# Kernel optimization log

Hardware: AMD Instinct MI355X
Metric: run time of the kernel (lower is better)

The kernel has to match this reference:

```python
import jax, jax.numpy as jnp
import numpy as np

NUM_HEADS = 8
HEAD_DIM = 32  # token_dim 256 / 8 heads


def setup_inputs() -> dict:
    key = jax.random.key(0)
    ks = jax.random.split(key, 12)
    Q, N, E, D, G = 8192, 65536, 262144, 256, 64
    query_tokens = jax.random.normal(ks[0], (Q, D), dtype=jnp.float32)
    support_feats = jax.random.normal(ks[1], (N, D), dtype=jnp.float32)
    geo_embed = jax.random.normal(ks[2], (Q, G), dtype=jnp.float32)
    q_idx = jnp.sort(jax.random.randint(ks[3], (E,), 0, Q, dtype=jnp.int32)).astype(jnp.int32)
    s_idx = jax.random.randint(ks[4], (E,), 0, N, dtype=jnp.int32)
    # fan-in scaled weights (nn.Linear-like init scale)
    Wq = jax.random.normal(ks[5], (D, D), dtype=jnp.float32) / np.sqrt(D)
    Wk = jax.random.normal(ks[6], (D, D), dtype=jnp.float32) / np.sqrt(D)
    Wv = jax.random.normal(ks[7], (D, D), dtype=jnp.float32) / np.sqrt(D)
    Wg = jax.random.normal(ks[8], (G, D), dtype=jnp.float32) / np.sqrt(G)
    Wo = jax.random.normal(ks[9], (D, D), dtype=jnp.float32) / np.sqrt(D)
    bo = jnp.zeros((D,), dtype=jnp.float32)
    log_tau = jnp.zeros((), dtype=jnp.float32)  # tau = 1.0
    return {"query_tokens": query_tokens, "support_feats": support_feats,
            "geo_embed": geo_embed, "q_idx": q_idx, "s_idx": s_idx,
            "num_queries": Q, "Wq": Wq, "Wk": Wk, "Wv": Wv, "Wg": Wg,
            "Wo": Wo, "bo": bo, "log_tau": log_tau}


def reference(query_tokens, support_feats, geo_embed, q_idx, s_idx, num_queries,
              Wq, Wk, Wv, Wg, Wo, bo, log_tau):
    H, Dh = NUM_HEADS, HEAD_DIM
    E = q_idx.shape[0]
    # dense projections on node features (done once per node, then gathered)
    Qf = query_tokens @ Wq            # [Q, D]
    Kf = support_feats @ Wk           # [N, D]
    Vf = support_feats @ Wv           # [N, D]
    Gf = geo_embed @ Wg               # [Q, D]
    q = Qf[q_idx].reshape(E, H, Dh)
    k = Kf[s_idx].reshape(E, H, Dh)
    v = Vf[s_idx].reshape(E, H, Dh)
    g = Gf[q_idx].reshape(E, H, Dh)
    tau = jnp.exp(log_tau)
    scores = jnp.sum(q * k, axis=-1) / (jnp.sqrt(jnp.float32(Dh)) * tau)  # [E, H]
    # segment softmax over ragged neighbor lists; torch scatter_reduce(amax)
    # starts from zeros with include_self=True -> max with 0
    smax = jnp.maximum(jax.ops.segment_max(scores, q_idx, num_segments=num_queries), 0.0)
    ex = jnp.exp(scores - smax[q_idx])
    ssum = jax.ops.segment_sum(ex, q_idx, num_segments=num_queries)
    alpha = ex / jnp.maximum(ssum[q_idx], 1e-8)                            # [E, H]
    weighted = alpha[..., None] * (v + g)                                  # [E, H, Dh]
    out = jax.ops.segment_sum(weighted, q_idx, num_segments=num_queries)   # [Q, H, Dh]
    out = out.reshape(num_queries, H * Dh)
    return out @ Wo + bo
```

## Files before the change

kernel.cpp:

```cpp
#include <hip/hip_runtime.h>
#include <hip/hip_bf16.h>
#include <hip/hip_fp8.h>

typedef __attribute__((ext_vector_type(8))) short short8v;
typedef __attribute__((ext_vector_type(4))) float f32x4;
typedef __attribute__((ext_vector_type(2))) float f32x2;

#define DEVFN __device__ __forceinline__

DEVFN unsigned short f2bf(float x) {
  __hip_bfloat16 h = __float2bfloat16(x);
  return *reinterpret_cast<unsigned short*>(&h);
}

DEVFN float bf2f(unsigned short u) {
  unsigned int x = ((unsigned int)u) << 16;
  float f;
  __builtin_memcpy(&f, &x, 4);
  return f;
}

DEVFN unsigned char f2fp8(float x) {
  __hip_fp8_e4m3 h(x);
  return *reinterpret_cast<unsigned char*>(&h);
}

#if __has_builtin(__builtin_amdgcn_cvt_pk_f32_fp8)
DEVFN void fp8x4_to_f32(unsigned int u, float* out) {
  f32x2 lo = __builtin_amdgcn_cvt_pk_f32_fp8(u, false);
  f32x2 hi = __builtin_amdgcn_cvt_pk_f32_fp8(u, true);
  out[0] = lo[0]; out[1] = lo[1]; out[2] = hi[0]; out[3] = hi[1];
}
#else
DEVFN float fp8_1_to_f32(unsigned int b) {
  const unsigned int s = (b >> 7) & 1, e = (b >> 3) & 15, m = b & 7;
  unsigned int bits = (s << 31) | ((e + 120) << 23) | (m << 20);
  float f;
  __builtin_memcpy(&f, &bits, 4);
  if (e == 0) f = (s ? -1.f : 1.f) * (float)m * 0.001953125f;
  return f;
}
DEVFN void fp8x4_to_f32(unsigned int u, float* out) {
  out[0] = fp8_1_to_f32(u & 0xff);
  out[1] = fp8_1_to_f32((u >> 8) & 0xff);
  out[2] = fp8_1_to_f32((u >> 16) & 0xff);
  out[3] = fp8_1_to_f32((u >> 24) & 0xff);
}
#endif

DEVFN void gload16(const void* g, void* l) {
  __builtin_amdgcn_global_load_lds(
      (const __attribute__((address_space(1))) void*)g,
      (__attribute__((address_space(3))) void*)l, 16, 0, 0);
}

__global__ __launch_bounds__(256) void prep(
    const float* __restrict__ Wk, const float* __restrict__ Wv,
    const float* __restrict__ Wq, const float* __restrict__ Wo,
    const float* __restrict__ Wg,
    unsigned short* __restrict__ Btkv, unsigned short* __restrict__ Btq,
    unsigned short* __restrict__ Bto, unsigned short* __restrict__ Btg,
    const int* __restrict__ q_idx, int* __restrict__ q_start, int Q, int E) {
  const int b = blockIdx.x, t = threadIdx.x;
  if (b < 256) {
    const int wi = b >> 6, bb = b & 63;
    const float* W = (wi == 0) ? Wk : (wi == 1) ? Wv : (wi == 2) ? Wq : Wo;
    unsigned short* O = (wi == 0) ? Btkv : (wi == 1) ? (Btkv + 65536)
                     : (wi == 2) ? Btq : Bto;
    for (int id = bb * 256 + t; id < 65536; id += 64 * 256) {
      const int n = id >> 8, k = id & 255;
      O[id] = f2bf(W[k * 256 + n]);
    }
  } else if (b < 272) {
    for (int id = (b - 256) * 256 + t; id < 16384; id += 16 * 256) {
      const int n = id >> 6, k = id & 63;
      Btg[id] = f2bf(Wg[k * 256 + n]);
    }
  } else {
    const int q = (b - 272) * 256 + t;
    if (q <= Q) {
      int lo = 0, hi = E;
      while (lo < hi) { int mid = (lo + hi) >> 1; if (q_idx[mid] < q) lo = mid + 1; else hi = mid; }
      q_start[q] = lo;
    }
  }
}

template <int KT, bool A_F32, int OUT_MODE, bool HAS_BIAS>
DEVFN void gemm_body(const void* __restrict__ Av,
                     const unsigned short* __restrict__ Bt,
                     void* __restrict__ Cv, const float* __restrict__ bias,
                     int ldc, int bid, int gx, int nwg,
                     unsigned short (*As)[128 * 32],
                     unsigned short (*Bs)[128 * 32]) {
  constexpr int K = KT * 32;

  const int t = threadIdx.x;
  const int wv = t >> 6, l = t & 63;
  const int wr = wv >> 1, wc = wv & 1;
  const int lr = l & 15, lk = l >> 4;

  const int swz = (bid & 7) * (nwg >> 3) + (bid >> 3);
  const int n0 = (swz % gx) * 128;
  const int m0 = (swz / gx) * 128;

  f32x4 acc[4][4];
#pragma unroll
  for (int m = 0; m < 4; ++m)
#pragma unroll
    for (int n = 0; n < 4; ++n) acc[m][n] = (f32x4){0.f, 0.f, 0.f, 0.f};

  const int wbase = (t & ~63) * 16;

  const int arow = t >> 1, ac0 = (t & 1) * 2;
  const float* Afp = A_F32 ? ((const float*)Av + (size_t)(m0 + arow) * K + ac0 * 8)
                           : nullptr;
  float4 reg0[4], reg1[4];

  auto loadA = [&](float4 (&rg)[4], int k0) {
    const float* p = Afp + k0;
#pragma unroll
    for (int j = 0; j < 4; ++j) rg[j] = *(const float4*)(p + j * 4);
  };
  auto writeA = [&](float4 (&rg)[4], int buf) {
    unsigned short u[16];
#pragma unroll
    for (int j = 0; j < 4; ++j) {
      u[4 * j + 0] = f2bf(rg[j].x); u[4 * j + 1] = f2bf(rg[j].y);
      u[4 * j + 2] = f2bf(rg[j].z); u[4 * j + 3] = f2bf(rg[j].w);
    }
    const int cs0 = ac0 ^ ((arow >> 1) & 3);
    const int cs1 = (ac0 + 1) ^ ((arow >> 1) & 3);
    *(short8v*)&As[buf][arow * 32 + cs0 * 8] = *(short8v*)&u[0];
    *(short8v*)&As[buf][arow * 32 + cs1 * 8] = *(short8v*)&u[8];
  };
  auto stageA_lds = [&](int buf, int k0) {
    const unsigned short* Ab = (const unsigned short*)Av;
#pragma unroll
    for (int s = 0; s < 2; ++s) {
      const int cidx = s * 256 + t;
      const int row = cidx >> 2, c = cidx & 3;
      const int cs = c ^ ((row >> 1) & 3);
      gload16(Ab + (size_t)(m0 + row) * K + k0 + cs * 8,
              (char*)&As[buf][0] + (size_t)s * 4096 + wbase);
    }
  };
  auto stageB = [&](int buf, int k0) {
#pragma unroll
    for (int s = 0; s < 2; ++s) {
      const int cidx = s * 256 + t;
      const int row = cidx >> 2, c = cidx & 3;
      const int cs = c ^ ((row >> 1) & 3);
      gload16(Bt + (size_t)(n0 + row) * K + k0 + cs * 8,
              (char*)&Bs[buf][0] + (size_t)s * 4096 + wbase);
    }
  };

  auto compute = [&](int buf) {
    short8v a[4], b[4];
#pragma unroll
    for (int m = 0; m < 4; ++m) {
      const int row = wr * 64 + m * 16 + lr;
      const int cs = lk ^ ((row >> 1) & 3);
      a[m] = *(const short8v*)&As[buf][row * 32 + cs * 8];
    }
#pragma unroll
    for (int n = 0; n < 4; ++n) {
      const int row = wc * 64 + n * 16 + lr;
      const int cs = lk ^ ((row >> 1) & 3);
      b[n] = *(const short8v*)&Bs[buf][row * 32 + cs * 8];
    }
#pragma unroll
    for (int m = 0; m < 4; ++m)
#pragma unroll
      for (int n = 0; n < 4; ++n)
        acc[m][n] = __builtin_amdgcn_mfma_f32_16x16x32_bf16(a[m], b[n], acc[m][n], 0, 0, 0);
  };

  stageB(0, 0);
  if (KT > 1) stageB(1, 32);
  if (A_F32) {
    loadA(reg0, 0);
    if (KT > 1) loadA(reg1, 32);
    writeA(reg0, 0);
  } else {
    stageA_lds(0, 0);
    if (KT > 1) stageA_lds(1, 32);
  }

#pragma unroll
  for (int tt = 0; tt < KT; ++tt) {
    __builtin_amdgcn_s_barrier();
    __builtin_amdgcn_sched_barrier(0);
    if (A_F32) {
      if (tt + 2 < KT) {
        if (((tt + 2) & 1) == 0) loadA(reg0, (tt + 2) * 32);
        else                     loadA(reg1, (tt + 2) * 32);
        stageB((tt + 2) % 3, (tt + 2) * 32);
      }
      if (tt + 1 < KT) {
        if (((tt + 1) & 1) == 0) writeA(reg0, (tt + 1) % 3);
        else                     writeA(reg1, (tt + 1) % 3);
      }
      if (tt < KT - 2)       asm volatile("s_waitcnt vmcnt(8) lgkmcnt(0)" ::: "memory");
      else if (tt == KT - 2) asm volatile("s_waitcnt vmcnt(2) lgkmcnt(0)" ::: "memory");
      else                   asm volatile("s_waitcnt vmcnt(0) lgkmcnt(0)" ::: "memory");
    } else {
      if (tt + 2 < KT) {
        stageA_lds((tt + 2) % 3, (tt + 2) * 32);
        stageB((tt + 2) % 3, (tt + 2) * 32);
      }
      const int rem = (tt + 2 < KT ? tt + 2 : KT - 1) - tt;
      if (rem >= 2)      asm volatile("s_waitcnt vmcnt(8)" ::: "memory");
      else if (rem == 1) asm volatile("s_waitcnt vmcnt(4)" ::: "memory");
      else               asm volatile("s_waitcnt vmcnt(0)" ::: "memory");
    }
    __builtin_amdgcn_s_barrier();
    __builtin_amdgcn_sched_barrier(0);
    compute(tt % 3);
  }

#pragma unroll
  for (int m = 0; m < 4; ++m)
#pragma unroll
    for (int n = 0; n < 4; ++n) {
      const f32x4 v = acc[m][n];
      const int col = n0 + wc * 64 + n * 16 + lr;
      const int rbase = m0 + wr * 64 + m * 16 + lk * 4;
      float bv = 0.f;
      if (HAS_BIAS) bv = bias[col];
#pragma unroll
      for (int r = 0; r < 4; ++r) {
        const float val = v[r] + bv;
        if (OUT_MODE == 0) {
          ((float*)Cv)[(size_t)(rbase + r) * ldc + col] = val;
        } else if (OUT_MODE == 1) {
          ((unsigned short*)Cv)[(size_t)(rbase + r) * ldc + col] = f2bf(val);
        } else {
          ((unsigned char*)Cv)[(size_t)(rbase + r) * 512 + col] = f2fp8(val);
        }
      }
    }
}

__global__ __launch_bounds__(256) void proj(
    const float* __restrict__ support, const float* __restrict__ query,
    const float* __restrict__ geo,
    const unsigned short* __restrict__ Btkv, const unsigned short* __restrict__ Btq,
    const unsigned short* __restrict__ Btg,
    unsigned char* __restrict__ KV, unsigned short* __restrict__ Qf,
    unsigned short* __restrict__ Gf) {
  __shared__ unsigned short As[3][128 * 32];
  __shared__ unsigned short Bs[3][128 * 32];
  const int b = blockIdx.x;
  if (b < 2048) {
    gemm_body<8, true, 2, false>(support, Btkv, KV, nullptr, 0, b, 4, 2048, As, Bs);
  } else if (b < 2176) {
    gemm_body<8, true, 1, false>(query, Btq, Qf, nullptr, 256, b - 2048, 2, 128, As, Bs);
  } else {
    gemm_body<2, true, 1, false>(geo, Btg, Gf, nullptr, 256, b - 2176, 2, 128, As, Bs);
  }
}

__global__ __launch_bounds__(256) void gemm_final(
    const unsigned short* __restrict__ A, const unsigned short* __restrict__ Bt,
    void* __restrict__ C, const float* __restrict__ bias) {
  __shared__ unsigned short As[3][128 * 32];
  __shared__ unsigned short Bs[3][128 * 32];
  gemm_body<8, false, 0, true>(A, Bt, C, bias, 256, blockIdx.x, 2, 128, As, Bs);
}

__global__ __launch_bounds__(256) void edge_attn(
    const int* __restrict__ s_idx, const int* __restrict__ q_start,
    const unsigned char* __restrict__ KVb, const unsigned short* __restrict__ Qf,
    const unsigned short* __restrict__ Gf, unsigned short* __restrict__ out_pre,
    const float* __restrict__ log_tau) {
  const int q = blockIdx.x;
  const int t = threadIdx.x;
  const int w = t >> 6;
  const int lane = t & 63;
  const int stream = w * 2 + (lane >> 5);
  const int sl = lane & 31;
  const int start = q_start[q], end = q_start[q + 1];

  const float tau = __expf(log_tau[0]);
  const float rs = 1.0f / (5.656854249492381f * tau);

  float qv[8];
  {
    uint4 qw = *(const uint4*)(Qf + (size_t)q * 256 + sl * 8);
    const unsigned int ws_[4] = {qw.x, qw.y, qw.z, qw.w};
#pragma unroll
    for (int j = 0; j < 4; ++j) {
      qv[2 * j]     = bf2f((unsigned short)(ws_[j] & 0xffffu)) * rs;
      qv[2 * j + 1] = bf2f((unsigned short)(ws_[j] >> 16)) * rs;
    }
  }

  float o[8];
#pragma unroll
  for (int j = 0; j < 8; ++j) o[j] = 0.f;
  float lsum_p = 0.f;

  __shared__ int sseg[1024];

  for (int cb = start; cb < end; cb += 1024) {
    const int nb = min(1024, end - cb);
    __syncthreads();
    for (int jj = t; jj < nb; jj += 256) sseg[jj] = s_idx[cb + jj];
    __syncthreads();

    int j = stream;
    uint2 kc = {}, kn = {}, vc = {}, vn = {};
    if (j < nb) {
      const unsigned char* bp = KVb + (size_t)sseg[j] * 512;
      kc = *(const uint2*)(bp + sl * 8);
      vc = *(const uint2*)(bp + 256 + sl * 8);
    }
    if (j + 8 < nb) {
      const unsigned char* bp = KVb + (size_t)sseg[j + 8] * 512;
      kn = *(const uint2*)(bp + sl * 8);
      vn = *(const uint2*)(bp + 256 + sl * 8);
    }
    while (j < nb) {
      const int j2 = j + 16;
      uint2 k2 = {}, v2 = {};
      if (j2 < nb) {
        const unsigned char* bp = KVb + (size_t)sseg[j2] * 512;
        k2 = *(const uint2*)(bp + sl * 8);
        v2 = *(const uint2*)(bp + 256 + sl * 8);
      }
      float kf[8];
      fp8x4_to_f32(kc.x, kf);
      fp8x4_to_f32(kc.y, kf + 4);
      float p = 0.f;
#pragma unroll
      for (int jj = 0; jj < 8; ++jj) p = fmaf(qv[jj], kf[jj], p);
      p += __shfl_xor(p, 1);
      p += __shfl_xor(p, 2);
      const float ew = __expf(p);
      lsum_p += ew;
      float vf[8];
      fp8x4_to_f32(vc.x, vf);
      fp8x4_to_f32(vc.y, vf + 4);
#pragma unroll
      for (int jj = 0; jj < 8; ++jj) o[jj] = fmaf(ew, vf[jj], o[jj]);
      j += 8;
      kc = kn; vc = vn;
      kn = k2; vn = v2;
    }
  }

  __shared__ float o_sh[8][256];
  __shared__ float l_sh[8][8];
  *(float4*)&o_sh[stream][sl * 8]     = (float4){o[0], o[1], o[2], o[3]};
  *(float4*)&o_sh[stream][sl * 8 + 4] = (float4){o[4], o[5], o[6], o[7]};
  if ((sl & 3) == 0) l_sh[stream][sl >> 2] = lsum_p;
  __syncthreads();

  float osum = 0.f, lsum = 0.f;
  const int h = t >> 5;
#pragma unroll
  for (int s = 0; s < 8; ++s) {
    osum += o_sh[s][t];
    lsum += l_sh[s][h];
  }
  const float inv = 1.0f / fmaxf(lsum, 1e-8f);
  float res = 0.f;
  if (end > start) res = osum * inv + (lsum * inv) * bf2f(Gf[(size_t)q * 256 + t]);
  out_pre[(size_t)q * 256 + t] = f2bf(res);
}

extern "C" void kernel_launch(void* const* d_in, const int* in_sizes, int n_in,
                              void* d_out, int out_size, void* d_ws, size_t ws_size,
                              hipStream_t stream) {
  const float* query   = (const float*)d_in[0];
  const float* support = (const float*)d_in[1];
  const float* geo     = (const float*)d_in[2];
  const int*   q_idx   = (const int*)d_in[3];
  const int*   s_idx   = (const int*)d_in[4];
  const float* Wq      = (const float*)d_in[6];
  const float* Wk      = (const float*)d_in[7];
  const float* Wv      = (const float*)d_in[8];
  const float* Wg      = (const float*)d_in[9];
  const float* Wo      = (const float*)d_in[10];
  const float* bo      = (const float*)d_in[11];
  const float* log_tau = (const float*)d_in[12];

  const int D = 256;
  const int Q = in_sizes[0] / D;
  const int N = in_sizes[1] / D;
  const int E = in_sizes[3];

  unsigned char* wsb = (unsigned char*)d_ws;
  unsigned char*  KV   = wsb;
  unsigned short* Qf   = (unsigned short*)(wsb + (size_t)N * 512);
  unsigned short* Gf   = Qf   + (size_t)Q * 256;
  unsigned short* Opre = Gf   + (size_t)Q * 256;
  unsigned short* Btkv = Opre + (size_t)Q * 256;
  unsigned short* Btq  = Btkv + 512 * 256;
  unsigned short* Btg  = Btq  + 256 * 256;
  unsigned short* Bto  = Btg  + 256 * 64;
  int* q_start = (int*)(Bto + 256 * 256);

  dim3 blk(256);

  prep<<<dim3(305), blk, 0, stream>>>(Wk, Wv, Wq, Wo, Wg,
                                      Btkv, Btq, Bto, Btg, q_idx, q_start, Q, E);

  proj<<<dim3(2304), blk, 0, stream>>>(support, query, geo, Btkv, Btq, Btg,
                                       KV, Qf, Gf);

  edge_attn<<<dim3(Q), blk, 0, stream>>>(s_idx, q_start, KV,
                                         Qf, Gf, Opre, log_tau);

  gemm_final<<<dim3(128), blk, 0, stream>>>(Opre, Bto, d_out, bo);
}
```

Measured before the change: 81.95 us.

## Restructure f32-input projection GEMM to process K-tiles in pairs per barrier

Splits the GEMM body into a dedicated f32-A projection path and a bf16-A final path. The projection GEMM now uses four LDS buffers and four register slots, staging two K-steps at a time and computing two tiles between barrier pairs, which halves the number of barriers per tile. The aim is less synchronisation overhead and deeper prefetch in the dominant projection kernel. In exchange it uses more LDS (4 buffers) and more registers, which may lower occupancy.

```diff
diff --git a/kernel.cpp b/kernel.cpp
--- a/kernel.cpp
+++ b/kernel.cpp
@@ -86,14 +86,15 @@
   }
 }
 
-template <int KT, bool A_F32, int OUT_MODE, bool HAS_BIAS>
-DEVFN void gemm_body(const void* __restrict__ Av,
-                     const unsigned short* __restrict__ Bt,
-                     void* __restrict__ Cv, const float* __restrict__ bias,
-                     int ldc, int bid, int gx, int nwg,
-                     unsigned short (*As)[128 * 32],
-                     unsigned short (*Bs)[128 * 32]) {
+template <int KT, int OUT_MODE>
+DEVFN void gemm_f32_paired(const float* __restrict__ A,
+                           const unsigned short* __restrict__ Bt,
+                           void* __restrict__ Cv,
+                           int ldc, int bid, int gx, int nwg,
+                           unsigned short (*As)[128 * 32],
+                           unsigned short (*Bs)[128 * 32]) {
   constexpr int K = KT * 32;
+  static_assert(KT % 2 == 0, "KT must be even");
 
   const int t = threadIdx.x;
   const int wv = t >> 6, l = t & 63;
@@ -111,11 +112,10 @@
     for (int n = 0; n < 4; ++n) acc[m][n] = (f32x4){0.f, 0.f, 0.f, 0.f};
 
   const int wbase = (t & ~63) * 16;
-
   const int arow = t >> 1, ac0 = (t & 1) * 2;
-  const float* Afp = A_F32 ? ((const float*)Av + (size_t)(m0 + arow) * K + ac0 * 8)
-                           : nullptr;
-  float4 reg0[4], reg1[4];
+  const float* Afp = A + (size_t)(m0 + arow) * K + ac0 * 8;
+
+  float4 rg0[4], rg1[4], rg2[4], rg3[4];
 
   auto loadA = [&](float4 (&rg)[4], int k0) {
     const float* p = Afp + k0;
@@ -134,16 +134,17 @@
     *(short8v*)&As[buf][arow * 32 + cs0 * 8] = *(short8v*)&u[0];
     *(short8v*)&As[buf][arow * 32 + cs1 * 8] = *(short8v*)&u[8];
   };
-  auto stageA_lds = [&](int buf, int k0) {
-    const unsigned short* Ab = (const unsigned short*)Av;
-#pragma unroll
-    for (int s = 0; s < 2; ++s) {
-      const int cidx = s * 256 + t;
-      const int row = cidx >> 2, c = cidx & 3;
-      const int cs = c ^ ((row >> 1) & 3);
-      gload16(Ab + (size_t)(m0 + row) * K + k0 + cs * 8,
-              (char*)&As[buf][0] + (size_t)s * 4096 + wbase);
-    }
+  auto loadSlot = [&](int slot, int k0) {
+    if (slot == 0) loadA(rg0, k0);
+    else if (slot == 1) loadA(rg1, k0);
+    else if (slot == 2) loadA(rg2, k0);
+    else loadA(rg3, k0);
+  };
+  auto writeSlot = [&](int slot, int buf) {
+    if (slot == 0) writeA(rg0, buf);
+    else if (slot == 1) writeA(rg1, buf);
+    else if (slot == 2) writeA(rg2, buf);
+    else writeA(rg3, buf);
   };
   auto stageB = [&](int buf, int k0) {
 #pragma unroll
@@ -155,7 +156,6 @@
               (char*)&Bs[buf][0] + (size_t)s * 4096 + wbase);
     }
   };
-
   auto compute = [&](int buf) {
     short8v a[4], b[4];
 #pragma unroll
@@ -178,43 +178,152 @@
   };
 
   stageB(0, 0);
-  if (KT > 1) stageB(1, 32);
-  if (A_F32) {
-    loadA(reg0, 0);
-    if (KT > 1) loadA(reg1, 32);
-    writeA(reg0, 0);
+  stageB(1, 32);
+  loadSlot(0, 0);
+  loadSlot(1, 32);
+  writeSlot(0, 0);
+  writeSlot(1, 1);
+  if (KT > 2) {
+    loadSlot(2, 64);
+    loadSlot(3, 96);
+    stageB(2, 64);
+    stageB(3, 96);
+    asm volatile("s_waitcnt vmcnt(12) lgkmcnt(0)" ::: "memory");
   } else {
-    stageA_lds(0, 0);
-    if (KT > 1) stageA_lds(1, 32);
-  }
+    asm volatile("s_waitcnt vmcnt(0) lgkmcnt(0)" ::: "memory");
+  }
+  __builtin_amdgcn_s_barrier();
+  __builtin_amdgcn_sched_barrier(0);
+
+#pragma unroll
+  for (int p = 0; p < KT / 2; ++p) {
+    compute((2 * p) % 4);
+    compute((2 * p + 1) % 4);
+    if (p + 1 < KT / 2) {
+      const int q = p + 1;
+      __builtin_amdgcn_s_barrier();
+      __builtin_amdgcn_sched_barrier(0);
+      if (2 * q + 2 < KT) {
+        loadSlot((2 * q + 2) & 3, (2 * q + 2) * 32);
+        loadSlot((2 * q + 3) & 3, (2 * q + 3) * 32);
+      }
+      writeSlot((2 * q) & 3, (2 * q) % 4);
+      writeSlot((2 * q + 1) & 3, (2 * q + 1) % 4);
+      if (2 * q + 2 < KT) {
+        stageB((2 * q + 2) % 4, (2 * q + 2) * 32);
+        stageB((2 * q + 3) % 4, (2 * q + 3) * 32);
+      }
+      if (2 * q + 2 < KT)
+        asm volatile("s_waitcnt vmcnt(12) lgkmcnt(0)" ::: "memory");
+      else
+        asm volatile("s_waitcnt vmcnt(0) lgkmcnt(0)" ::: "memory");
+      __builtin_amdgcn_s_barrier();
+      __builtin_amdgcn_sched_barrier(0);
+    }
+  }
+
+#pragma unroll
+  for (int m = 0; m < 4; ++m)
+#pragma unroll
+    for (int n = 0; n < 4; ++n) {
+      const f32x4 v = acc[m][n];
+      const int col = n0 + wc * 64 + n * 16 + lr;
+      const int rbase = m0 + wr * 64 + m * 16 + lk * 4;
+#pragma unroll
+      for (int r = 0; r < 4; ++r) {
+        const float val = v[r];
+        if (OUT_MODE == 1) {
+          ((unsigned short*)Cv)[(size_t)(rbase + r) * ldc + col] = f2bf(val);
+        } else {
+          ((unsigned char*)Cv)[(size_t)(rbase + r) * 512 + col] = f2fp8(val);
+        }
+      }
+    }
+}
+
+template <int KT, bool HAS_BIAS>
+DEVFN void gemm_bf16_body(const unsigned short* __restrict__ A,
+                          const unsigned short* __restrict__ Bt,
+                          float* __restrict__ Cv, const float* __restrict__ bias,
+                          int ldc, int bid, int gx, int nwg,
+                          unsigned short (*As)[128 * 32],
+                          unsigned short (*Bs)[128 * 32]) {
+  constexpr int K = KT * 32;
+
+  const int t = threadIdx.x;
+  const int wv = t >> 6, l = t & 63;
+  const int wr = wv >> 1, wc = wv & 1;
+  const int lr = l & 15, lk = l >> 4;
+
+  const int swz = (bid & 7) * (nwg >> 3) + (bid >> 3);
+  const int n0 = (swz % gx) * 128;
+  const int m0 = (swz / gx) * 128;
+
+  f32x4 acc[4][4];
+#pragma unroll
+  for (int m = 0; m < 4; ++m)
+#pragma unroll
+    for (int n = 0; n < 4; ++n) acc[m][n] = (f32x4){0.f, 0.f, 0.f, 0.f};
+
+  const int wbase = (t & ~63) * 16;
+
+  auto stageA = [&](int buf, int k0) {
+#pragma unroll
+    for (int s = 0; s < 2; ++s) {
+      const int cidx = s * 256 + t;
+      const int row = cidx >> 2, c = cidx & 3;
+      const int cs = c ^ ((row >> 1) & 3);
+      gload16(A + (size_t)(m0 + row) * K + k0 + cs * 8,
+              (char*)&As[buf][0] + (size_t)s * 4096 + wbase);
+    }
+  };
+  auto stageB = [&](int buf, int k0) {
+#pragma unroll
+    for (int s = 0; s < 2; ++s) {
+      const int cidx = s * 256 + t;
+      const int row = cidx >> 2, c = cidx & 3;
+      const int cs = c ^ ((row >> 1) & 3);
+      gload16(Bt + (size_t)(n0 + row) * K + k0 + cs * 8,
+              (char*)&Bs[buf][0] + (size_t)s * 4096 + wbase);
+    }
+  };
+  auto compute = [&](int buf) {
+    short8v a[4], b[4];
+#pragma unroll
+    for (int m = 0; m < 4; ++m) {
+      const int row = wr * 64 + m * 16 + lr;
+      const int cs = lk ^ ((row >> 1) & 3);
+      a[m] = *(const short8v*)&As[buf][row * 32 + cs * 8];
+    }
+#pragma unroll
+    for (int n = 0; n < 4; ++n) {
+      const int row = wc * 64 + n * 16 + lr;
+      const int cs = lk ^ ((row >> 1) & 3);
+      b[n] = *(const short8v*)&Bs[buf][row * 32 + cs * 8];
+    }
+#pragma unroll
+    for (int m = 0; m < 4; ++m)
+#pragma unroll
+      for (int n = 0; n < 4; ++n)
+        acc[m][n] = __builtin_amdgcn_mfma_f32_16x16x32_bf16(a[m], b[n], acc[m][n], 0, 0, 0);
+  };
+
+  stageA(0, 0);
+  stageB(0, 0);
+  if (KT > 1) { stageA(1, 32); stageB(1, 32); }
 
 #pragma unroll
   for (int tt = 0; tt < KT; ++tt) {
     __builtin_amdgcn_s_barrier();
     __builtin_amdgcn_sched_barrier(0);
-    if (A_F32) {
-      if (tt + 2 < KT) {
-        if (((tt + 2) & 1) == 0) loadA(reg0, (tt + 2) * 32);
-        else                     loadA(reg1, (tt + 2) * 32);
-        stageB((tt + 2) % 3, (tt + 2) * 32);
-      }
-      if (tt + 1 < KT) {
-        if (((tt + 1) & 1) == 0) writeA(reg0, (tt + 1) % 3);
-        else                     writeA(reg1, (tt + 1) % 3);
-      }
-      if (tt < KT - 2)       asm volatile("s_waitcnt vmcnt(8) lgkmcnt(0)" ::: "memory");
-      else if (tt == KT - 2) asm volatile("s_waitcnt vmcnt(2) lgkmcnt(0)" ::: "memory");
-      else                   asm volatile("s_waitcnt vmcnt(0) lgkmcnt(0)" ::: "memory");
-    } else {
-      if (tt + 2 < KT) {
-        stageA_lds((tt + 2) % 3, (tt + 2) * 32);
-        stageB((tt + 2) % 3, (tt + 2) * 32);
-      }
-      const int rem = (tt + 2 < KT ? tt + 2 : KT - 1) - tt;
-      if (rem >= 2)      asm volatile("s_waitcnt vmcnt(8)" ::: "memory");
-      else if (rem == 1) asm volatile("s_waitcnt vmcnt(4)" ::: "memory");
-      else               asm volatile("s_waitcnt vmcnt(0)" ::: "memory");
-    }
+    if (tt + 2 < KT) {
+      stageA((tt + 2) % 3, (tt + 2) * 32);
+      stageB((tt + 2) % 3, (tt + 2) * 32);
+    }
+    const int rem = (tt + 2 < KT ? tt + 2 : KT - 1) - tt;
+    if (rem >= 2)      asm volatile("s_waitcnt vmcnt(8)" ::: "memory");
+    else if (rem == 1) asm volatile("s_waitcnt vmcnt(4)" ::: "memory");
+    else               asm volatile("s_waitcnt vmcnt(0)" ::: "memory");
     __builtin_amdgcn_s_barrier();
     __builtin_amdgcn_sched_barrier(0);
     compute(tt % 3);
@@ -230,16 +339,8 @@
       float bv = 0.f;
       if (HAS_BIAS) bv = bias[col];
 #pragma unroll
-      for (int r = 0; r < 4; ++r) {
-        const float val = v[r] + bv;
-        if (OUT_MODE == 0) {
-          ((float*)Cv)[(size_t)(rbase + r) * ldc + col] = val;
-        } else if (OUT_MODE == 1) {
-          ((unsigned short*)Cv)[(size_t)(rbase + r) * ldc + col] = f2bf(val);
-        } else {
-          ((unsigned char*)Cv)[(size_t)(rbase + r) * 512 + col] = f2fp8(val);
-        }
-      }
+      for (int r = 0; r < 4; ++r)
+        Cv[(size_t)(rbase + r) * ldc + col] = v[r] + bv;
     }
 }
 
@@ -250,24 +351,24 @@
     const unsigned short* __restrict__ Btg,
     unsigned char* __restrict__ KV, unsigned short* __restrict__ Qf,
     unsigned short* __restrict__ Gf) {
+  __shared__ unsigned short As[4][128 * 32];
+  __shared__ unsigned short Bs[4][128 * 32];
+  const int b = blockIdx.x;
+  if (b < 2048) {
+    gemm_f32_paired<8, 2>(support, Btkv, KV, 0, b, 4, 2048, As, Bs);
+  } else if (b < 2176) {
+    gemm_f32_paired<8, 1>(query, Btq, Qf, 256, b - 2048, 2, 128, As, Bs);
+  } else {
+    gemm_f32_paired<2, 1>(geo, Btg, Gf, 256, b - 2176, 2, 128, As, Bs);
+  }
+}
+
+__global__ __launch_bounds__(256) void gemm_final(
+    const unsigned short* __restrict__ A, const unsigned short* __restrict__ Bt,
+    float* __restrict__ C, const float* __restrict__ bias) {
   __shared__ unsigned short As[3][128 * 32];
   __shared__ unsigned short Bs[3][128 * 32];
-  const int b = blockIdx.x;
-  if (b < 2048) {
-    gemm_body<8, true, 2, false>(support, Btkv, KV, nullptr, 0, b, 4, 2048, As, Bs);
-  } else if (b < 2176) {
-    gemm_body<8, true, 1, false>(query, Btq, Qf, nullptr, 256, b - 2048, 2, 128, As, Bs);
-  } else {
-    gemm_body<2, true, 1, false>(geo, Btg, Gf, nullptr, 256, b - 2176, 2, 128, As, Bs);
-  }
-}
-
-__global__ __launch_bounds__(256) void gemm_final(
-    const unsigned short* __restrict__ A, const unsigned short* __restrict__ Bt,
-    void* __restrict__ C, const float* __restrict__ bias) {
-  __shared__ unsigned short As[3][128 * 32];
-  __shared__ unsigned short Bs[3][128 * 32];
-  gemm_body<8, false, 0, true>(A, Bt, C, bias, 256, blockIdx.x, 2, 128, As, Bs);
+  gemm_bf16_body<8, true>(A, Bt, C, bias, 256, blockIdx.x, 2, 128, As, Bs);
 }
 
 __global__ __launch_bounds__(256) void edge_attn(
@@ -414,5 +515,5 @@
   edge_attn<<<dim3(Q), blk, 0, stream>>>(s_idx, q_start, KV,
                                          Qf, Gf, Opre, log_tau);
 
-  gemm_final<<<dim3(128), blk, 0, stream>>>(Opre, Bto, d_out, bo);
-}
+  gemm_final<<<dim3(128), blk, 0, stream>>>(Opre, Bto, (float*)d_out, bo);
+}
```

After: 85.05 us. 1.04x slower.

## Keep full fp32 support row-tile in LDS across all KV output column tiles

Applied to the files above, without the earlier changes.

The K/V projection now gives each workgroup one 128-row tile of support features and loops over all four 128-column output tiles. The whole 128x256 A tile is converted to bf16 once and held in LDS (32K shorts), so the fp32 support matrix is read from global memory once instead of four times. Only the B tile is double-buffered per step. The cost is a larger LDS footprint (80KB per block), which lowers occupancy, and fewer workgroups (512 instead of 2048) for the KV part.

```diff
diff --git a/kernel.cpp b/kernel.cpp
--- a/kernel.cpp
+++ b/kernel.cpp
@@ -86,6 +86,138 @@
   }
 }
 
+DEVFN void gemm_kv_persist(const float* __restrict__ A,
+                           const unsigned short* __restrict__ Bt,
+                           unsigned char* __restrict__ KV,
+                           int bid, int nwg,
+                           unsigned short (*As)[128 * 32],
+                           unsigned short (*Bs)[128 * 32]) {
+  constexpr int K = 256;
+  const int t = threadIdx.x;
+  const int wv = t >> 6, l = t & 63;
+  const int wr = wv >> 1, wc = wv & 1;
+  const int lr = l & 15, lk = l >> 4;
+
+  const int swz = (bid & 7) * (nwg >> 3) + (bid >> 3);
+  const int m0 = swz * 128;
+
+  const int wbase = (t & ~63) * 16;
+  const int arow = t >> 1, ac0 = (t & 1) * 2;
+  const float* Afp = A + (size_t)(m0 + arow) * K + ac0 * 8;
+
+  f32x4 acc[4][4];
+#pragma unroll
+  for (int m = 0; m < 4; ++m)
+#pragma unroll
+    for (int n = 0; n < 4; ++n) acc[m][n] = (f32x4){0.f, 0.f, 0.f, 0.f};
+
+  float4 reg0[4], reg1[4];
+
+  auto loadA = [&](float4 (&rg)[4], int k0) {
+    const float* p = Afp + k0;
+#pragma unroll
+    for (int j = 0; j < 4; ++j) rg[j] = *(const float4*)(p + j * 4);
+  };
+  auto writeA = [&](float4 (&rg)[4], int tile) {
+    unsigned short u[16];
+#pragma unroll
+    for (int j = 0; j < 4; ++j) {
+      u[4 * j + 0] = f2bf(rg[j].x); u[4 * j + 1] = f2bf(rg[j].y);
+      u[4 * j + 2] = f2bf(rg[j].z); u[4 * j + 3] = f2bf(rg[j].w);
+    }
+    const int cs0 = ac0 ^ ((arow >> 1) & 3);
+    const int cs1 = (ac0 + 1) ^ ((arow >> 1) & 3);
+    *(short8v*)&As[tile][arow * 32 + cs0 * 8] = *(short8v*)&u[0];
+    *(short8v*)&As[tile][arow * 32 + cs1 * 8] = *(short8v*)&u[8];
+  };
+  auto loadSlot = [&](int tile) {
+    if ((tile & 1) == 0) loadA(reg0, tile * 32);
+    else                 loadA(reg1, tile * 32);
+  };
+  auto writeSlot = [&](int tile) {
+    if ((tile & 1) == 0) writeA(reg0, tile);
+    else                 writeA(reg1, tile);
+  };
+  auto stageB = [&](int buf, int p, int k0) {
+#pragma unroll
+    for (int s = 0; s < 2; ++s) {
+      const int cidx = s * 256 + t;
+      const int row = cidx >> 2, c = cidx & 3;
+      const int cs = c ^ ((row >> 1) & 3);
+      gload16(Bt + (size_t)(p * 128 + row) * K + k0 + cs * 8,
+              (char*)&Bs[buf][0] + (size_t)s * 4096 + wbase);
+    }
+  };
+  auto compute = [&](int atile, int bbuf) {
+    short8v a[4], b[4];
+#pragma unroll
+    for (int m = 0; m < 4; ++m) {
+      const int row = wr * 64 + m * 16 + lr;
+      const int cs = lk ^ ((row >> 1) & 3);
+      a[m] = *(const short8v*)&As[atile][row * 32 + cs * 8];
+    }
+#pragma unroll
+    for (int n = 0; n < 4; ++n) {
+      const int row = wc * 64 + n * 16 + lr;
+      const int cs = lk ^ ((row >> 1) & 3);
+      b[n] = *(const short8v*)&Bs[bbuf][row * 32 + cs * 8];
+    }
+#pragma unroll
+    for (int m = 0; m < 4; ++m)
+#pragma unroll
+      for (int n = 0; n < 4; ++n)
+        acc[m][n] = __builtin_amdgcn_mfma_f32_16x16x32_bf16(a[m], b[n], acc[m][n], 0, 0, 0);
+  };
+
+  stageB(0, 0, 0);
+  loadSlot(0);
+  loadSlot(1);
+  writeSlot(0);
+  asm volatile("s_waitcnt lgkmcnt(0)" ::: "memory");
+  __builtin_amdgcn_s_barrier();
+  __builtin_amdgcn_sched_barrier(0);
+
+#pragma unroll
+  for (int i = 0; i < 32; ++i) {
+    if (i > 0) {
+      __builtin_amdgcn_s_barrier();
+      __builtin_amdgcn_sched_barrier(0);
+    }
+    if (i < 8) {
+      if (i + 1 < 8) writeSlot(i + 1);
+      stageB((i + 1) & 1, (i + 1) >> 3, ((i + 1) & 7) * 32);
+      if (i + 2 < 8) loadSlot(i + 2);
+      if (i == 7) asm volatile("s_waitcnt vmcnt(2) lgkmcnt(0)" ::: "memory");
+      else        asm volatile("s_waitcnt lgkmcnt(0)" ::: "memory");
+    } else {
+      if (i + 1 < 32) {
+        stageB((i + 1) & 1, (i + 1) >> 3, ((i + 1) & 7) * 32);
+        asm volatile("s_waitcnt vmcnt(2)" ::: "memory");
+      } else {
+        asm volatile("s_waitcnt vmcnt(0)" ::: "memory");
+      }
+    }
+    __builtin_amdgcn_s_barrier();
+    __builtin_amdgcn_sched_barrier(0);
+    compute(i & 7, i & 1);
+    if ((i & 7) == 7) {
+      const int p = i >> 3;
+#pragma unroll
+      for (int m = 0; m < 4; ++m)
+#pragma unroll
+        for (int n = 0; n < 4; ++n) {
+          const f32x4 v = acc[m][n];
+          const int col = p * 128 + wc * 64 + n * 16 + lr;
+          const int rbase = m0 + wr * 64 + m * 16 + lk * 4;
+#pragma unroll
+          for (int r = 0; r < 4; ++r)
+            KV[(size_t)(rbase + r) * 512 + col] = f2fp8(v[r]);
+          acc[m][n] = (f32x4){0.f, 0.f, 0.f, 0.f};
+        }
+    }
+  }
+}
+
 template <int KT, bool A_F32, int OUT_MODE, bool HAS_BIAS>
 DEVFN void gemm_body(const void* __restrict__ Av,
                      const unsigned short* __restrict__ Bt,
@@ -111,7 +243,6 @@
     for (int n = 0; n < 4; ++n) acc[m][n] = (f32x4){0.f, 0.f, 0.f, 0.f};
 
   const int wbase = (t & ~63) * 16;
-
   const int arow = t >> 1, ac0 = (t & 1) * 2;
   const float* Afp = A_F32 ? ((const float*)Av + (size_t)(m0 + arow) * K + ac0 * 8)
                            : nullptr;
@@ -234,10 +365,8 @@
         const float val = v[r] + bv;
         if (OUT_MODE == 0) {
           ((float*)Cv)[(size_t)(rbase + r) * ldc + col] = val;
-        } else if (OUT_MODE == 1) {
+        } else {
           ((unsigned short*)Cv)[(size_t)(rbase + r) * ldc + col] = f2bf(val);
-        } else {
-          ((unsigned char*)Cv)[(size_t)(rbase + r) * 512 + col] = f2fp8(val);
         }
       }
     }
@@ -250,15 +379,20 @@
     const unsigned short* __restrict__ Btg,
     unsigned char* __restrict__ KV, unsigned short* __restrict__ Qf,
     unsigned short* __restrict__ Gf) {
-  __shared__ unsigned short As[3][128 * 32];
-  __shared__ unsigned short Bs[3][128 * 32];
+  __shared__ unsigned short LDSU[40960];
   const int b = blockIdx.x;
-  if (b < 2048) {
-    gemm_body<8, true, 2, false>(support, Btkv, KV, nullptr, 0, b, 4, 2048, As, Bs);
-  } else if (b < 2176) {
-    gemm_body<8, true, 1, false>(query, Btq, Qf, nullptr, 256, b - 2048, 2, 128, As, Bs);
+  if (b < 512) {
+    gemm_kv_persist(support, Btkv, KV, b, 512,
+                    (unsigned short (*)[128 * 32])&LDSU[0],
+                    (unsigned short (*)[128 * 32])&LDSU[32768]);
+  } else if (b < 640) {
+    gemm_body<8, true, 1, false>(query, Btq, Qf, nullptr, 256, b - 512, 2, 128,
+                                 (unsigned short (*)[128 * 32])&LDSU[0],
+                                 (unsigned short (*)[128 * 32])&LDSU[12288]);
   } else {
-    gemm_body<2, true, 1, false>(geo, Btg, Gf, nullptr, 256, b - 2176, 2, 128, As, Bs);
+    gemm_body<2, true, 1, false>(geo, Btg, Gf, nullptr, 256, b - 640, 2, 128,
+                                 (unsigned short (*)[128 * 32])&LDSU[0],
+                                 (unsigned short (*)[128 * 32])&LDSU[12288]);
   }
 }
 
@@ -408,8 +542,8 @@
   prep<<<dim3(305), blk, 0, stream>>>(Wk, Wv, Wq, Wo, Wg,
                                       Btkv, Btq, Bto, Btg, q_idx, q_start, Q, E);
 
-  proj<<<dim3(2304), blk, 0, stream>>>(support, query, geo, Btkv, Btq, Btg,
-                                       KV, Qf, Gf);
+  proj<<<dim3(768), blk, 0, stream>>>(support, query, geo, Btkv, Btq, Btg,
+                                      KV, Qf, Gf);
 
   edge_attn<<<dim3(Q), blk, 0, stream>>>(s_idx, q_start, KV,
                                          Qf, Gf, Opre, log_tau);
```

New measurement: 76.00 us, median of 2. 7.3% less time.
